# Performance work log

Hardware: AMD Instinct MI355X
Metric: run time of the kernel (lower is better)

## Reference

```python
import jax, jax.numpy as jnp
import numpy as np

B, T, DMODEL = 2, 2048, 1024
H, DK, DV = 16, 64, 64
FF = 4096
EPS = 1e-5


def _layernorm_2d(x):
    # torch LayerNorm(normalized_shape=(T, dmodel)): normalize jointly over last two
    # dims, biased variance, weight=1 / bias=0 (freshly constructed each forward).
    mu = jnp.mean(x, axis=(1, 2), keepdims=True)
    var = jnp.mean((x - mu) ** 2, axis=(1, 2), keepdims=True)
    return (x - mu) / jnp.sqrt(var + EPS)


def setup_inputs() -> dict:
    key = jax.random.key(0)
    ks = jax.random.split(key, 9)
    s = 0.02  # small init for numerical sanity (original uses uniform(-1,1))
    return {
        "x": jax.random.normal(ks[0], (B, T, DMODEL), jnp.float32),
        "Wq": jax.random.normal(ks[1], (H, DMODEL, DK), jnp.float32) * s,
        "Wk": jax.random.normal(ks[2], (H, DMODEL, DK), jnp.float32) * s,
        "Wv": jax.random.normal(ks[3], (H, DMODEL, DV), jnp.float32) * s,
        "Wo": jax.random.normal(ks[4], (DMODEL, DMODEL), jnp.float32) * s,
        "W1": jax.random.normal(ks[5], (DMODEL, FF), jnp.float32) * s,
        "b1": jnp.zeros((FF,), jnp.float32),
        "W2": jax.random.normal(ks[6], (FF, DMODEL), jnp.float32) * s,
        "b2": jnp.zeros((DMODEL,), jnp.float32),
    }


def reference(x, Wq, Wk, Wv, Wo, W1, b1, W2, b2):
    b, t, d = x.shape
    h, _, dk = Wq.shape
    dv = Wv.shape[-1]
    # per-head projections: (B,H,T,dk/dv)
    Qp = jnp.einsum("btd,hdk->bhtk", x, Wq)
    Kp = jnp.einsum("btd,hdk->bhtk", x, Wk)
    Vp = jnp.einsum("btd,hdv->bhtv", x, Wv)
    scores = jnp.einsum("bhqk,bhsk->bhqs", Qp, Kp) / np.sqrt(dk).astype(np.float32)
    # NOTE: original does torch.softmax(heads, 2) -> softmax over the QUERY axis
    attn = jax.nn.softmax(scores, axis=2)
    heads = jnp.einsum("bhqs,bhsv->bqhv", attn, Vp).reshape(b, t, h * dv)
    att_out = heads @ Wo
    o1 = _layernorm_2d(x + att_out)
    ff = jnp.maximum(o1 @ W1 + b1, 0.0) @ W2 + b2
    return _layernorm_2d(o1 + ff)
```

## Files before the change

### kernel.cpp

```cpp
#include <hip/hip_runtime.h>
#include <hip/hip_bf16.h>
#include <cstddef>
#include <cstdint>

typedef __hip_bfloat16 hbf;
typedef __attribute__((ext_vector_type(8))) __bf16 bf16x8;
typedef __attribute__((ext_vector_type(4))) float f32x4;

#define B_ 2
#define T_ 2048
#define D_ 1024
#define H_ 16
#define FF_ 4096
#define EPS_ 1e-5f
#define SCALE_ 0.18033688011112f

__device__ __forceinline__ float bf2f(hbf v) { return __bfloat162float(v); }
__device__ __forceinline__ float fexp2(float x) {
  return __builtin_amdgcn_exp2f(x);
}
__device__ __forceinline__ float flog2(float x) {
  return __builtin_amdgcn_logf(x);
}
__device__ __forceinline__ float ldin(const void* p, size_t i, int isbf) {
  return isbf ? __bfloat162float(((const hbf*)p)[i]) : ((const float*)p)[i];
}
__device__ __forceinline__ void ston(void* p, size_t i, float v, int isbf) {
  if (isbf) ((hbf*)p)[i] = __float2bfloat16(v);
  else ((float*)p)[i] = v;
}
__device__ __forceinline__ f32x4 mfma16(bf16x8 a, bf16x8 b, f32x4 c) {
  return __builtin_amdgcn_mfma_f32_16x16x32_bf16(a, b, c, 0, 0, 0);
}
__device__ __forceinline__ bf16x8 ldfrag(const hbf* p) {
  return *(const bf16x8*)p;
}
__device__ __forceinline__ void glds16(const hbf* g, hbf* l) {
  __builtin_amdgcn_global_load_lds(
      (const __attribute__((address_space(1))) void*)g,
      (__attribute__((address_space(3))) void*)l, 16, 0, 0);
}

__global__ __launch_bounds__(256) void detect_dtype(const unsigned* x,
                                                    int* flag) {
  __shared__ int cnt[256];
  int c = 0;
  for (int i = threadIdx.x; i < 4096; i += 256) {
    unsigned low = x[i] & 0xFFFFu;
    unsigned e = (low >> 7) & 0xFFu;
    if (e >= 100u && e <= 142u) c++;
  }
  cnt[threadIdx.x] = c;
  __syncthreads();
  for (int off = 128; off > 0; off >>= 1) {
    if ((int)threadIdx.x < off) cnt[threadIdx.x] += cnt[threadIdx.x + off];
    __syncthreads();
  }
  if (threadIdx.x == 0) *flag = (cnt[0] > 2458) ? 1 : 0;
}

__device__ __forceinline__ void tr_tile(const void* __restrict__ src,
                                        hbf* __restrict__ dst, int R, int C,
                                        size_t zoff, int cx, int ry, int f,
                                        float (*tile)[33]) {
  const int tx = threadIdx.x & 31, ty = threadIdx.x >> 5;
  const int c0 = cx * 32, r0 = ry * 32;
#pragma unroll
  for (int p = 0; p < 4; p++) {
    int rr = p * 8 + ty;
    tile[rr][tx] = ldin(src, zoff + (size_t)(r0 + rr) * C + c0 + tx, f);
  }
  __syncthreads();
#pragma unroll
  for (int p = 0; p < 4; p++) {
    int cc = p * 8 + ty;
    dst[zoff + (size_t)(c0 + cc) * R + r0 + tx] = __float2bfloat16(tile[tx][cc]);
  }
}

__global__ __launch_bounds__(256) void preconv(
    const void* __restrict__ x, const void* __restrict__ Wq,
    const void* __restrict__ Wk, const void* __restrict__ Wv,
    const void* __restrict__ Wo, const void* __restrict__ W1,
    const void* __restrict__ W2, const void* __restrict__ b1,
    const void* __restrict__ b2, hbf* __restrict__ xb,
    hbf* __restrict__ wqkvt, hbf* __restrict__ wot, hbf* __restrict__ w1t,
    hbf* __restrict__ w2t, hbf* __restrict__ b1b, hbf* __restrict__ b2b,
    const int* __restrict__ flag) {
  __shared__ float tile[32][33];
  const int f = *flag;
  const int bid = blockIdx.x;
  if (bid < 3072) {
    int which = bid >> 10;
    int r = bid & 1023;
    int z = r >> 6, rem = r & 63;
    int ry = rem >> 1, cx = rem & 1;
    const void* src = (which == 0) ? Wq : (which == 1) ? Wk : Wv;
    hbf* dst = wqkvt + (size_t)which * (D_ * D_);
    tr_tile(src, dst, 1024, 64, (size_t)z * 65536, cx, ry, f, tile);
  } else if (bid < 4096) {
    int t = bid - 3072;
    tr_tile(Wo, wot, 1024, 1024, 0, t & 31, t >> 5, f, tile);
  } else if (bid < 8192) {
    int t = bid - 4096;
    tr_tile(W1, w1t, 1024, 4096, 0, t & 127, t >> 7, f, tile);
  } else if (bid < 12288) {
    int t = bid - 8192;
    tr_tile(W2, w2t, 4096, 1024, 0, t & 31, t >> 5, f, tile);
  } else if (bid < 13312) {
    size_t base = (size_t)(bid - 12288) * 4096;
    for (int i = threadIdx.x; i < 4096; i += 256)
      xb[base + i] = __float2bfloat16(ldin(x, base + i, f));
  } else if (bid == 13312) {
    for (int i = threadIdx.x; i < FF_; i += 256)
      b1b[i] = __float2bfloat16(ldin(b1, i, f));
  } else {
    for (int i = threadIdx.x; i < D_; i += 256)
      b2b[i] = __float2bfloat16(ldin(b2, i, f));
  }
}

template <int MODE, int BM, int BN>
__global__ __launch_bounds__(256) void gemm_bt(
    const hbf* __restrict__ A, const hbf* __restrict__ Bt, hbf* __restrict__ C,
    float* __restrict__ Cf0, float* __restrict__ Cf1,
    const hbf* __restrict__ e1, float* __restrict__ red, int M, int N, int K,
    int LDK) {
  constexpr int WM = BM / 2, WN = BN / 2;
  constexpr int IF = WM / 16, JF = WN / 16;
  __shared__ alignas(16) hbf As[BM * 64];
  __shared__ alignas(16) hbf Bs[BN * 64];
  const int tid = threadIdx.x;
  const int wave = tid >> 6, lane = tid & 63;
  const int quad = lane >> 4, l16 = lane & 15;
  const int m0 = blockIdx.y * BM, n0 = blockIdx.x * BN;
  const int mw = (wave >> 1) * WM, nw = (wave & 1) * WN;
  const int srow = tid >> 3;
  const int scol = (tid & 7) * 8;
  const int kbase = (MODE == 4) ? blockIdx.z * K : 0;
  const f32x4 zero = {0.f, 0.f, 0.f, 0.f};
  f32x4 acc[IF][JF];
#pragma unroll
  for (int i = 0; i < IF; i++)
#pragma unroll
    for (int j = 0; j < JF; j++) acc[i][j] = zero;

  const hbf* ga = &A[(size_t)(m0 + srow) * LDK + kbase + scol];
  const hbf* gb = &Bt[(size_t)(n0 + srow) * LDK + kbase + scol];
  hbf* lA = &As[wave * 512];
  hbf* lB = &Bs[wave * 512];

  for (int k0 = 0; k0 < K; k0 += 64) {
#pragma unroll
    for (int c = 0; c < BM / 32; c++)
      glds16(ga + (size_t)(c * 32) * LDK + k0, lA + c * 2048);
#pragma unroll
    for (int c = 0; c < BN / 32; c++)
      glds16(gb + (size_t)(c * 32) * LDK + k0, lB + c * 2048);
    __syncthreads();
    bf16x8 af[2][IF], bfr[2][JF];
#pragma unroll
    for (int h = 0; h < 2; h++) {
#pragma unroll
      for (int i = 0; i < IF; i++)
        af[h][i] = ldfrag(&As[(mw + i * 16 + l16) * 64 + h * 32 + quad * 8]);
#pragma unroll
      for (int j = 0; j < JF; j++)
        bfr[h][j] = ldfrag(&Bs[(nw + j * 16 + l16) * 64 + h * 32 + quad * 8]);
    }
#pragma unroll
    for (int h = 0; h < 2; h++)
#pragma unroll
      for (int i = 0; i < IF; i++)
#pragma unroll
        for (int j = 0; j < JF; j++)
          acc[i][j] = mfma16(af[h][i], bfr[h][j], acc[i][j]);
    __syncthreads();
  }
  float ssum = 0.f, ssq = 0.f;
#pragma unroll
  for (int i = 0; i < IF; i++)
#pragma unroll
    for (int j = 0; j < JF; j++)
#pragma unroll
      for (int r = 0; r < 4; r++) {
        int m = m0 + mw + i * 16 + quad * 4 + r;
        int n = n0 + nw + j * 16 + l16;
        float v = acc[i][j][r];
        if (MODE == 0) {
          int which = n >> 10, n1 = n & 1023;
          int h = n1 >> 6, cc = n1 & 63;
          int b = m >> 11, t = m & (T_ - 1);
          if (which == 0) v *= SCALE_;
          C[(size_t)which * ((size_t)B_ * H_ * T_ * 64) +
            (((size_t)(b * H_ + h)) * T_ + t) * 64 + cc] = __float2bfloat16(v);
        } else if (MODE == 1) {
          hbf hv = __float2bfloat16(v + bf2f(e1[(size_t)m * N + n]));
          C[(size_t)m * N + n] = hv;
          float fv = bf2f(hv);
          ssum += fv;
          ssq += fv * fv;
        } else if (MODE == 2) {
          C[(size_t)m * N + n] = __float2bfloat16(fmaxf(v + bf2f(e1[n]), 0.f));
        } else if (MODE == 4) {
          float* Cf = blockIdx.z ? Cf1 : Cf0;
          Cf[(size_t)m * N + n] = v;
        }
      }
  if (MODE == 1) {
    float* sc = (float*)As;
    sc[tid] = ssum;
    sc[256 + tid] = ssq;
    __syncthreads();
    for (int off = 128; off > 0; off >>= 1) {
      if (tid < off) {
        sc[tid] += sc[tid + off];
        sc[256 + tid] += sc[256 + tid + off];
      }
      __syncthreads();
    }
    if (tid == 0) {
      int b = m0 >> 11;
      atomicAdd(&red[b * 2 + 0], sc[0]);
      atomicAdd(&red[b * 2 + 1], sc[256]);
    }
  }
}

__global__ __launch_bounds__(256) void attn_stats(const hbf* __restrict__ Q,
                                                  const hbf* __restrict__ K,
                                                  const hbf* __restrict__ V,
                                                  hbf* __restrict__ Vt) {
  __shared__ alignas(16) hbf Ks[64 * 72];
  __shared__ alignas(16) hbf Qs[64 * 72];
  __shared__ float sAdj[64];
  const int bh = blockIdx.y;
  const int s0 = blockIdx.x * 64;
  const int tid = threadIdx.x;
  const int wave = tid >> 6, lane = tid & 63;
  const int quad = lane >> 4, l16 = lane & 15;
  const int sw = wave * 16;
  const hbf* Kb = K + (size_t)bh * T_ * 64;
  const hbf* Qb = Q + (size_t)bh * T_ * 64;
  const hbf* Vb = V + (size_t)bh * T_ * 64;
  hbf* Vtb = Vt + (size_t)bh * 64 * T_;
  const int r_ = tid >> 3, c_ = (tid & 7) * 8;
#pragma unroll
  for (int c = 0; c < 2; c++) {
    int row = c * 32 + r_;
    *(float4*)(&Ks[row * 72 + c_]) =
        *(const float4*)(&Kb[(size_t)(s0 + row) * 64 + c_]);
  }
  __syncthreads();
  bf16x8 kf0 = ldfrag(&Ks[(sw + l16) * 72 + quad * 8]);
  bf16x8 kf1 = ldfrag(&Ks[(sw + l16) * 72 + 32 + quad * 8]);
  float m_thr[4], l_thr[4];
#pragma unroll
  for (int r = 0; r < 4; r++) {
    m_thr[r] = -1e30f;
    l_thr[r] = 0.f;
  }
  const f32x4 zero = {0.f, 0.f, 0.f, 0.f};
  for (int qt = 0; qt < T_ / 64; qt++) {
    if (qt) __syncthreads();
#pragma unroll
    for (int c = 0; c < 2; c++) {
      int row = c * 32 + r_;
      *(float4*)(&Qs[row * 72 + c_]) =
          *(const float4*)(&Qb[(size_t)(qt * 64 + row) * 64 + c_]);
    }
    __syncthreads();
    f32x4 acc[4];
#pragma unroll
    for (int j = 0; j < 4; j++) {
      bf16x8 qf0 = ldfrag(&Qs[(j * 16 + l16) * 72 + quad * 8]);
      bf16x8 qf1 = ldfrag(&Qs[(j * 16 + l16) * 72 + 32 + quad * 8]);
      f32x4 a = zero;
      a = mfma16(kf0, qf0, a);
      a = mfma16(kf1, qf1, a);
      acc[j] = a;
    }
#pragma unroll
    for (int r = 0; r < 4; r++) {
      float mt = fmaxf(fmaxf(acc[0][r], acc[1][r]),
                       fmaxf(acc[2][r], acc[3][r]));
      float nm = fmaxf(m_thr[r], mt);
      float s = l_thr[r] * fexp2(m_thr[r] - nm);
#pragma unroll
      for (int j = 0; j < 4; j++) s += fexp2(acc[j][r] - nm);
      l_thr[r] = s;
      m_thr[r] = nm;
    }
  }
#pragma unroll
  for (int d = 1; d < 16; d <<= 1) {
#pragma unroll
    for (int r = 0; r < 4; r++) {
      float om = __shfl_xor(m_thr[r], d);
      float ol = __shfl_xor(l_thr[r], d);
      float nm = fmaxf(m_thr[r], om);
      l_thr[r] = l_thr[r] * fexp2(m_thr[r] - nm) + ol * fexp2(om - nm);
      m_thr[r] = nm;
    }
  }
  if (l16 == 0) {
#pragma unroll
    for (int r = 0; r < 4; r++)
      sAdj[sw + quad * 4 + r] = m_thr[r] + flog2(l_thr[r]);
  }
  __syncthreads();
#pragma unroll
  for (int c = 0; c < 2; c++) {
    int e = (c * 256 + tid) * 8;
    int r = e >> 6, col = e & 63;
    union alignas(16) {
      hbf h[8];
      float4 f4;
    } u;
    u.f4 = *(const float4*)(&Vb[(size_t)(s0 + r) * 64 + col]);
    float sc = fexp2(-sAdj[r]);
#pragma unroll
    for (int k2 = 0; k2 < 8; k2++)
      u.h[k2] = __float2bfloat16(bf2f(u.h[k2]) * sc);
    *(float4*)(&Ks[r * 72 + col]) = u.f4;
  }
  __syncthreads();
#pragma unroll
  for (int c = 0; c < 2; c++) {
    int e = (c * 256 + tid) * 8;
    int v = e >> 6, tt = e & 63;
    union alignas(16) {
      hbf h[8];
      float4 f4;
    } u;
#pragma unroll
    for (int k2 = 0; k2 < 8; k2++) u.h[k2] = Ks[(tt + k2) * 72 + v];
    *(float4*)(&Vtb[(size_t)v * T_ + s0 + tt]) = u.f4;
  }
}

__global__ __launch_bounds__(256) void attn_apply(const hbf* __restrict__ Q,
                                                  const hbf* __restrict__ K,
                                                  const hbf* __restrict__ Vt,
                                                  hbf* __restrict__ heads) {
  __shared__ alignas(16) hbf P2[4 * 2 * 16 * 72];
  const int bh = blockIdx.y;
  const int b = bh >> 4, h = bh & 15;
  const int q0 = blockIdx.x * 128;
  const int tid = threadIdx.x;
  const int wave = tid >> 6, lane = tid & 63;
  const int quad = lane >> 4, l16 = lane & 15;
  const int qw = wave * 32;
  const hbf* Qb = Q + (size_t)bh * T_ * 64;
  const hbf* Kb = K + (size_t)bh * T_ * 64;
  const hbf* Vtb = Vt + (size_t)bh * 64 * T_;
  hbf* Pw = &P2[wave * (2 * 16 * 72)];
  const f32x4 zero = {0.f, 0.f, 0.f, 0.f};
  bf16x8 qf[2][2];
#pragma unroll
  for (int i = 0; i < 2; i++)
#pragma unroll
    for (int hh = 0; hh < 2; hh++)
      qf[i][hh] = ldfrag(&Qb[(size_t)(q0 + qw + i * 16 + l16) * 64 + hh * 32 +
                             quad * 8]);
  f32x4 accO[2][4];
#pragma unroll
  for (int i = 0; i < 2; i++)
#pragma unroll
    for (int j = 0; j < 4; j++) accO[i][j] = zero;

  for (int st = 0; st < T_ / 64; st++) {
    const hbf* Kt = &Kb[(size_t)(st * 64 + l16) * 64 + quad * 8];
    bf16x8 kf[4][2];
#pragma unroll
    for (int j = 0; j < 4; j++)
#pragma unroll
      for (int hh = 0; hh < 2; hh++)
        kf[j][hh] = ldfrag(Kt + j * (16 * 64) + hh * 32);
    f32x4 accS[2][4];
#pragma unroll
    for (int i = 0; i < 2; i++)
#pragma unroll
      for (int j = 0; j < 4; j++) {
        f32x4 a = mfma16(kf[j][0], qf[i][0], zero);
        accS[i][j] = mfma16(kf[j][1], qf[i][1], a);
      }
#pragma unroll
    for (int i = 0; i < 2; i++)
#pragma unroll
      for (int j = 0; j < 4; j++) {
        union {
          hbf h4[4];
          uint2 u;
        } pk;
#pragma unroll
        for (int r = 0; r < 4; r++)
          pk.h4[r] = __float2bfloat16(fexp2(accS[i][j][r]));
        *(uint2*)&Pw[i * (16 * 72) + l16 * 72 + j * 16 + quad * 4] = pk.u;
      }
    bf16x8 pf[2][2], vf[4][2];
#pragma unroll
    for (int i = 0; i < 2; i++)
#pragma unroll
      for (int hh = 0; hh < 2; hh++)
        pf[i][hh] =
            ldfrag(&Pw[i * (16 * 72) + l16 * 72 + hh * 32 + quad * 8]);
#pragma unroll
    for (int j2 = 0; j2 < 4; j2++)
#pragma unroll
      for (int hh = 0; hh < 2; hh++)
        vf[j2][hh] = ldfrag(&Vtb[(size_t)(j2 * 16 + l16) * T_ + st * 64 +
                                 hh * 32 + quad * 8]);
#pragma unroll
    for (int i = 0; i < 2; i++)
#pragma unroll
      for (int j2 = 0; j2 < 4; j2++) {
        accO[i][j2] = mfma16(pf[i][0], vf[j2][0], accO[i][j2]);
        accO[i][j2] = mfma16(pf[i][1], vf[j2][1], accO[i][j2]);
      }
  }
#pragma unroll
  for (int i = 0; i < 2; i++)
#pragma unroll
    for (int j2 = 0; j2 < 4; j2++)
#pragma unroll
      for (int r = 0; r < 4; r++) {
        int q = q0 + qw + i * 16 + quad * 4 + r;
        int v = j2 * 16 + l16;
        heads[((size_t)(b * T_ + q)) * D_ + h * 64 + v] =
            __float2bfloat16(accO[i][j2][r]);
      }
}

__global__ __launch_bounds__(256) void ln_norm(const hbf* __restrict__ src,
                                               const float* __restrict__ red,
                                               void* dst,
                                               const int* __restrict__ flag,
                                               int force_bf) {
  const int isbf = force_bf ? 1 : *flag;
  const float invN = 1.f / (float)(T_ * D_);
  for (size_t i = (size_t)blockIdx.x * 256 + threadIdx.x;
       i < (size_t)B_ * T_ * D_; i += (size_t)gridDim.x * 256) {
    int b = (int)(i >> 21);
    float mu = red[b * 2 + 0] * invN;
    float var = red[b * 2 + 1] * invN - mu * mu;
    ston(dst, i, (bf2f(src[i]) - mu) * rsqrtf(var + EPS_), isbf);
  }
}

__global__ __launch_bounds__(256) void ln2_stats(const float* __restrict__ P0,
                                                 const float* __restrict__ P1,
                                                 const hbf* __restrict__ o1,
                                                 const hbf* __restrict__ b2b,
                                                 float* __restrict__ red) {
  __shared__ float s1[256], s2[256];
  const int b = blockIdx.y;
  const size_t base = (size_t)b * (T_ * D_);
  float sum = 0.f, sq = 0.f;
  for (size_t i = (size_t)blockIdx.x * 256 + threadIdx.x; i < (size_t)T_ * D_;
       i += (size_t)gridDim.x * 256) {
    size_t e = base + i;
    float v = P0[e] + P1[e] + bf2f(b2b[i & (D_ - 1)]) + bf2f(o1[e]);
    sum += v;
    sq += v * v;
  }
  s1[threadIdx.x] = sum;
  s2[threadIdx.x] = sq;
  __syncthreads();
  for (int off = 128; off > 0; off >>= 1) {
    if ((int)threadIdx.x < off) {
      s1[threadIdx.x] += s1[threadIdx.x + off];
      s2[threadIdx.x] += s2[threadIdx.x + off];
    }
    __syncthreads();
  }
  if (threadIdx.x == 0) {
    atomicAdd(&red[b * 2 + 0], s1[0]);
    atomicAdd(&red[b * 2 + 1], s2[0]);
  }
}

__global__ __launch_bounds__(256) void ln2_norm(
    const float* __restrict__ P0, const float* __restrict__ P1,
    const hbf* __restrict__ o1, const hbf* __restrict__ b2b,
    const float* __restrict__ red, void* dst, const int* __restrict__ flag) {
  const int isbf = *flag;
  const float invN = 1.f / (float)(T_ * D_);
  for (size_t i = (size_t)blockIdx.x * 256 + threadIdx.x;
       i < (size_t)B_ * T_ * D_; i += (size_t)gridDim.x * 256) {
    int b = (int)(i >> 21);
    float mu = red[b * 2 + 0] * invN;
    float var = red[b * 2 + 1] * invN - mu * mu;
    float v = P0[i] + P1[i] + bf2f(b2b[i & (D_ - 1)]) + bf2f(o1[i]);
    ston(dst, i, (v - mu) * rsqrtf(var + EPS_), isbf);
  }
}

extern "C" void kernel_launch(void* const* d_in, const int* in_sizes, int n_in,
                              void* d_out, int out_size, void* d_ws,
                              size_t ws_size, hipStream_t stream) {
  const void* x = d_in[0];
  const void* Wq = d_in[1];
  const void* Wk = d_in[2];
  const void* Wv = d_in[3];
  const void* Wo = d_in[4];
  const void* W1 = d_in[5];
  const void* W2 = d_in[7];
  const void* b1 = d_in[6];
  const void* b2 = d_in[8];

  const size_t MB = 1024 * 1024;
  if (ws_size < 89 * MB) return;

  char* w = (char*)d_ws;
  hbf* xb = (hbf*)(w + 0 * MB);
  hbf* wqkvt = (hbf*)(w + 8 * MB);
  hbf* wot = (hbf*)(w + 14 * MB);
  hbf* w1t = (hbf*)(w + 16 * MB);
  hbf* w2t = (hbf*)(w + 24 * MB);
  hbf* Qb = (hbf*)(w + 32 * MB);
  hbf* Kb = (hbf*)(w + 40 * MB);
  hbf* Vb = (hbf*)(w + 48 * MB);
  hbf* Vtb = (hbf*)(w + 56 * MB);
  hbf* heads = (hbf*)(w + 64 * MB);
  hbf* r1 = (hbf*)(w + 72 * MB);
  hbf* o1 = (hbf*)(w + 80 * MB);
  hbf* ff1 = (hbf*)(w + 32 * MB);
  float* P0 = (float*)(w + 0 * MB);
  float* P1 = (float*)(w + 64 * MB);
  hbf* b1b = (hbf*)(w + 88 * MB);
  hbf* b2b = b1b + FF_;
  float* red = (float*)(b2b + D_);
  int* flag = (int*)(red + 8);

  hipMemsetAsync(red, 0, 8 * sizeof(float) + sizeof(int), stream);
  detect_dtype<<<1, 256, 0, stream>>>((const unsigned*)x, flag);

  const int M = B_ * T_;
  preconv<<<13314, 256, 0, stream>>>(x, Wq, Wk, Wv, Wo, W1, W2, b1, b2, xb,
                                     wqkvt, wot, w1t, w2t, b1b, b2b, flag);
  gemm_bt<0, 128, 128><<<dim3(24, 32), 256, 0, stream>>>(
      xb, wqkvt, Qb, nullptr, nullptr, nullptr, nullptr, M, 3 * D_, D_, D_);
  attn_stats<<<dim3(32, 32), 256, 0, stream>>>(Qb, Kb, Vb, Vtb);
  attn_apply<<<dim3(16, 32), 256, 0, stream>>>(Qb, Kb, Vtb, heads);
  gemm_bt<1, 128, 64><<<dim3(16, 32), 256, 0, stream>>>(
      heads, wot, r1, nullptr, nullptr, xb, red, M, D_, D_, D_);
  ln_norm<<<4096, 256, 0, stream>>>(r1, red, o1, flag, 1);
  gemm_bt<2, 128, 128><<<dim3(32, 32), 256, 0, stream>>>(
      o1, w1t, ff1, nullptr, nullptr, b1b, nullptr, M, FF_, D_, D_);
  gemm_bt<4, 128, 128><<<dim3(8, 32, 2), 256, 0, stream>>>(
      ff1, w2t, nullptr, P0, P1, nullptr, nullptr, M, D_, FF_ / 2, FF_);
  ln2_stats<<<dim3(256, B_), 256, 0, stream>>>(P0, P1, o1, b2b, red + 4);
  ln2_norm<<<2048, 256, 0, stream>>>(P0, P1, o1, b2b, red + 4, d_out, flag);
}
```

Before: 528.1 us.

## Double-buffer K/V tiles in LDS with async global-to-LDS loads in attn_apply

The attention-apply kernel no longer has every wave load its own K and V fragments straight from global memory. The block now cooperatively stages each 64-row K tile and V^T tile into shared memory with global-to-LDS loads, using an XOR swizzle and two buffers. The next tile is fetched while the current one is consumed, so the four waves share one copy instead of each loading the same data. The cost is more LDS use and a block-wide barrier on every iteration, which may limit occupancy and add synchronisation stalls.

```diff
diff --git a/kernel.cpp b/kernel.cpp
--- a/kernel.cpp
+++ b/kernel.cpp
@@ -343,7 +343,9 @@
                                                   const hbf* __restrict__ K,
                                                   const hbf* __restrict__ Vt,
                                                   hbf* __restrict__ heads) {
-  __shared__ alignas(16) hbf P2[4 * 2 * 16 * 72];
+  __shared__ alignas(16) hbf Ksb[2 * 64 * 64];
+  __shared__ alignas(16) hbf Vsb[2 * 64 * 64];
+  __shared__ alignas(16) hbf Ps[4 * 32 * 72];
   const int bh = blockIdx.y;
   const int b = bh >> 4, h = bh & 15;
   const int q0 = blockIdx.x * 128;
@@ -354,8 +356,14 @@
   const hbf* Qb = Q + (size_t)bh * T_ * 64;
   const hbf* Kb = K + (size_t)bh * T_ * 64;
   const hbf* Vtb = Vt + (size_t)bh * 64 * T_;
-  hbf* Pw = &P2[wave * (2 * 16 * 72)];
-  const f32x4 zero = {0.f, 0.f, 0.f, 0.f};
+  hbf* Pw = &Ps[wave * 32 * 72];
+  const int srow = tid >> 3, sc8 = tid & 7;
+  const int swz = sc8 ^ (srow & 7);
+  const hbf* gk = Kb + (size_t)srow * 64 + swz * 8;
+  const hbf* gv = Vtb + (size_t)srow * T_ + swz * 8;
+  hbf* lK = &Ksb[wave * 512];
+  hbf* lV = &Vsb[wave * 512];
+  const int sx = (l16 & 7) * 8;
   bf16x8 qf[2][2];
 #pragma unroll
   for (int i = 0; i < 2; i++)
@@ -363,20 +371,37 @@
     for (int hh = 0; hh < 2; hh++)
       qf[i][hh] = ldfrag(&Qb[(size_t)(q0 + qw + i * 16 + l16) * 64 + hh * 32 +
                              quad * 8]);
+  const f32x4 zero = {0.f, 0.f, 0.f, 0.f};
   f32x4 accO[2][4];
 #pragma unroll
   for (int i = 0; i < 2; i++)
 #pragma unroll
     for (int j = 0; j < 4; j++) accO[i][j] = zero;
 
+  glds16(gk, lK);
+  glds16(gk + 2048, lK + 2048);
+  glds16(gv, lV);
+  glds16(gv + (size_t)32 * T_, lV + 2048);
+  __syncthreads();
+
   for (int st = 0; st < T_ / 64; st++) {
-    const hbf* Kt = &Kb[(size_t)(st * 64 + l16) * 64 + quad * 8];
+    const int cur = st & 1, nxt = cur ^ 1;
+    if (st < T_ / 64 - 1) {
+      size_t ko = (size_t)(st + 1) * 4096;
+      glds16(gk + ko, lK + nxt * 4096);
+      glds16(gk + ko + 2048, lK + nxt * 4096 + 2048);
+      glds16(gv + (st + 1) * 64, lV + nxt * 4096);
+      glds16(gv + (size_t)32 * T_ + (st + 1) * 64, lV + nxt * 4096 + 2048);
+    }
+    const hbf* Kc = &Ksb[cur * 4096];
+    const hbf* Vc = &Vsb[cur * 4096];
     bf16x8 kf[4][2];
 #pragma unroll
     for (int j = 0; j < 4; j++)
 #pragma unroll
       for (int hh = 0; hh < 2; hh++)
-        kf[j][hh] = ldfrag(Kt + j * (16 * 64) + hh * 32);
+        kf[j][hh] =
+            ldfrag(&Kc[(j * 16 + l16) * 64 + ((hh * 32 + quad * 8) ^ sx)]);
     f32x4 accS[2][4];
 #pragma unroll
     for (int i = 0; i < 2; i++)
@@ -396,28 +421,25 @@
 #pragma unroll
         for (int r = 0; r < 4; r++)
           pk.h4[r] = __float2bfloat16(fexp2(accS[i][j][r]));
-        *(uint2*)&Pw[i * (16 * 72) + l16 * 72 + j * 16 + quad * 4] = pk.u;
+        *(uint2*)&Pw[(i * 16 + l16) * 72 + j * 16 + quad * 4] = pk.u;
       }
-    bf16x8 pf[2][2], vf[4][2];
+    bf16x8 pf[2][2];
 #pragma unroll
     for (int i = 0; i < 2; i++)
 #pragma unroll
       for (int hh = 0; hh < 2; hh++)
-        pf[i][hh] =
-            ldfrag(&Pw[i * (16 * 72) + l16 * 72 + hh * 32 + quad * 8]);
-#pragma unroll
-    for (int j2 = 0; j2 < 4; j2++)
-#pragma unroll
-      for (int hh = 0; hh < 2; hh++)
-        vf[j2][hh] = ldfrag(&Vtb[(size_t)(j2 * 16 + l16) * T_ + st * 64 +
-                                 hh * 32 + quad * 8]);
-#pragma unroll
-    for (int i = 0; i < 2; i++)
-#pragma unroll
-      for (int j2 = 0; j2 < 4; j2++) {
-        accO[i][j2] = mfma16(pf[i][0], vf[j2][0], accO[i][j2]);
-        accO[i][j2] = mfma16(pf[i][1], vf[j2][1], accO[i][j2]);
+        pf[i][hh] = ldfrag(&Pw[(i * 16 + l16) * 72 + hh * 32 + quad * 8]);
+#pragma unroll
+    for (int j2 = 0; j2 < 4; j2++) {
+      bf16x8 vf0 = ldfrag(&Vc[(j2 * 16 + l16) * 64 + ((quad * 8) ^ sx)]);
+      bf16x8 vf1 = ldfrag(&Vc[(j2 * 16 + l16) * 64 + ((32 + quad * 8) ^ sx)]);
+#pragma unroll
+      for (int i = 0; i < 2; i++) {
+        accO[i][j2] = mfma16(pf[i][0], vf0, accO[i][j2]);
+        accO[i][j2] = mfma16(pf[i][1], vf1, accO[i][j2]);
       }
+    }
+    __syncthreads();
   }
 #pragma unroll
   for (int i = 0; i < 2; i++)
```

After: 461.8 us. 1.14x faster.
